# Kernel optimization log

Hardware: AMD Instinct MI355X
Metric: run time of the kernel (lower is better)

The kernel has to match this reference:

```python
import jax, jax.numpy as jnp
import numpy as np

D_MODEL = 1024
N_HEAD = 16
B, T = 4, 2048


def setup_inputs() -> dict:
    key = jax.random.key(0)
    k1, k2, k3, k4, k5 = jax.random.split(key, 5)
    s = 0.02
    return {
        "x": jax.random.normal(k1, (B, T, D_MODEL), dtype=jnp.float32),
        "w_attn": jax.random.normal(k2, (3 * D_MODEL, D_MODEL), dtype=jnp.float32) * s,
        "b_attn": jax.random.normal(k3, (3 * D_MODEL,), dtype=jnp.float32) * s,
        "w_proj": jax.random.normal(k4, (D_MODEL, D_MODEL), dtype=jnp.float32) * s,
        "b_proj": jax.random.normal(k5, (D_MODEL,), dtype=jnp.float32) * s,
    }


def reference(x, w_attn, b_attn, w_proj, b_proj):
    # x: [B, T, C]
    Bb, Tt, C = x.shape
    H = N_HEAD
    dk = C // H
    scale = 1.0 / np.sqrt(dk).astype(np.float32)

    qkv = x @ w_attn.T + b_attn                      # [B, T, 3C]
    q, k, v = jnp.split(qkv, 3, axis=-1)             # each [B, T, C]
    # -> [B, H, T, dk]
    q = q.reshape(Bb, Tt, H, dk).transpose(0, 2, 1, 3)
    k = k.reshape(Bb, Tt, H, dk).transpose(0, 2, 1, 3)
    v = v.reshape(Bb, Tt, H, dk).transpose(0, 2, 1, 3)

    att = jnp.einsum("bhqd,bhkd->bhqk", q, k) * scale   # [B, H, T, T]
    att = jax.nn.softmax(att, axis=-1)
    y = jnp.einsum("bhqk,bhkd->bhqd", att, v)            # [B, H, T, dk]
    y = y.transpose(0, 2, 1, 3).reshape(Bb, Tt, C)       # [B, T, C]
    return y @ w_proj.T + b_proj
```

## Files before the change

### kernel.cpp

```cpp
#include <hip/hip_runtime.h>
#include <hip/hip_bf16.h>

typedef __attribute__((ext_vector_type(8))) short short8;
typedef __attribute__((ext_vector_type(4))) float floatx4;
typedef __attribute__((ext_vector_type(16))) float floatx16;

#define B_ 4
#define T_ 2048
#define C_ 1024
#define H_ 16
#define DK_ 64
#define M_ (B_ * T_)
#define N3_ (3 * C_)

#define QSCALE 0.1803368801111243f

__device__ __forceinline__ unsigned short f2bf(float f) {
    union { float f; unsigned u; } v; v.f = f;
    unsigned r = v.u + 0x7fffu + ((v.u >> 16) & 1u);
    return (unsigned short)(r >> 16);
}
__device__ __forceinline__ unsigned fbits(float f) {
    union { float f; unsigned u; } v; v.f = f; return v.u;
}
__device__ __forceinline__ unsigned pack_bf16(float a, float b) {
#if __has_builtin(__builtin_amdgcn_cvt_pk_bf16_f32)
    typedef __attribute__((ext_vector_type(2))) __bf16 bf16x2;
    bf16x2 r = __builtin_amdgcn_cvt_pk_bf16_f32(a, b);
    union { bf16x2 v; unsigned u; } c; c.v = r; return c.u;
#else
    return __builtin_amdgcn_perm(fbits(b) + 0x8000u, fbits(a) + 0x8000u, 0x07060302u);
#endif
}

__device__ __forceinline__ void gload_lds16(const unsigned short* g, unsigned short* l) {
    __builtin_amdgcn_global_load_lds(
        (const __attribute__((address_space(1))) unsigned int*)(const void*)g,
        (__attribute__((address_space(3))) unsigned int*)(void*)l, 16, 0, 0);
}

#define NX4 (M_ * C_ / 4)
#define NA4 (N3_ * C_ / 4)
#define NP4 (C_ * C_ / 4)
__global__ __launch_bounds__(256) void cast3_kernel(const float* __restrict__ x,
                                                    const float* __restrict__ wa,
                                                    const float* __restrict__ wp,
                                                    unsigned short* __restrict__ xb,
                                                    unsigned short* __restrict__ wab,
                                                    unsigned short* __restrict__ wpb) {
    int i = blockIdx.x * 256 + threadIdx.x;
    const float* src; unsigned short* dst; int j;
    if (i < NX4) { src = x; dst = xb; j = i; }
    else if (i < NX4 + NA4) { src = wa; dst = wab; j = i - NX4; }
    else { src = wp; dst = wpb; j = i - NX4 - NA4; }
    float4 v = ((const float4*)src)[j];
    ushort4 o;
    o.x = f2bf(v.x); o.y = f2bf(v.y); o.z = f2bf(v.z); o.w = f2bf(v.w);
    ((ushort4*)dst)[j] = o;
}

#define BM 128
#define BN 128
#define BK 32

__global__ __launch_bounds__(256) void gemm_qkv(const unsigned short* __restrict__ A,
                                                const unsigned short* __restrict__ W,
                                                const float* __restrict__ bias,
                                                unsigned short* __restrict__ qout,
                                                unsigned short* __restrict__ kout,
                                                unsigned short* __restrict__ vout) {
    const int Kd = C_;
    __shared__ unsigned short As[BM * BK];
    __shared__ unsigned short Bs[BN * BK];
    int m0 = blockIdx.y * BM;
    int n0 = blockIdx.x * BN;
    int tid = threadIdx.x;
    int lane = tid & 63, w = tid >> 6;
    int wm = (w >> 1) * 64, wn = (w & 1) * 64;
    int l16 = lane & 15, quad = lane >> 4;
    int r4 = lane >> 2, c4 = (lane & 3) * 8;

    floatx4 acc[4][4] = {};
    for (int kt = 0; kt < Kd; kt += BK) {
        __syncthreads();
        for (int t = 0; t < 2; ++t) {
            int rbase = w * 32 + t * 16;
            gload_lds16(&A[(size_t)(m0 + rbase + r4) * Kd + kt + c4], &As[rbase * BK]);
            gload_lds16(&W[(size_t)(n0 + rbase + r4) * Kd + kt + c4], &Bs[rbase * BK]);
        }
        __syncthreads();
        short8 af[4], bf[4];
        for (int i = 0; i < 4; ++i)
            af[i] = *(const short8*)&As[(wm + 16 * i + l16) * BK + quad * 8];
        for (int j = 0; j < 4; ++j)
            bf[j] = *(const short8*)&Bs[(wn + 16 * j + l16) * BK + quad * 8];
        for (int i = 0; i < 4; ++i)
            for (int j = 0; j < 4; ++j)
                acc[i][j] = __builtin_amdgcn_mfma_f32_16x16x32_bf16(af[i], bf[j], acc[i][j], 0, 0, 0);
    }
    for (int i = 0; i < 4; ++i)
        for (int j = 0; j < 4; ++j) {
            int col = n0 + wn + 16 * j + l16;
            float bval = bias[col];
            int sec = col >> 10, cc = col & 1023;
            int h = cc >> 6, d = cc & 63;
            float qs = (sec == 0) ? QSCALE : 1.0f;
            unsigned short* dst = (sec == 0) ? qout : ((sec == 1) ? kout : vout);
            for (int r = 0; r < 4; ++r) {
                int m = m0 + wm + 16 * i + quad * 4 + r;
                int b = m >> 11, t = m & (T_ - 1);
                int bh = b * H_ + h;
                dst[((size_t)bh * T_ + t) * DK_ + d] = f2bf((acc[i][j][r] + bval) * qs);
            }
        }
}

__global__ __launch_bounds__(256) void gemm_proj(const unsigned short* __restrict__ A,
                                                 const unsigned short* __restrict__ W,
                                                 const float* __restrict__ bias,
                                                 float* __restrict__ out) {
    const int Kd = C_;
    __shared__ unsigned short As[BM * BK];
    __shared__ unsigned short Bs[BN * BK];
    int m0 = blockIdx.y * BM;
    int n0 = blockIdx.x * BN;
    int tid = threadIdx.x;
    int lane = tid & 63, w = tid >> 6;
    int wm = (w >> 1) * 64, wn = (w & 1) * 64;
    int l16 = lane & 15, quad = lane >> 4;
    int r4 = lane >> 2, c4 = (lane & 3) * 8;

    floatx4 acc[4][4] = {};
    for (int kt = 0; kt < Kd; kt += BK) {
        __syncthreads();
        for (int t = 0; t < 2; ++t) {
            int rbase = w * 32 + t * 16;
            gload_lds16(&A[(size_t)(m0 + rbase + r4) * Kd + kt + c4], &As[rbase * BK]);
            gload_lds16(&W[(size_t)(n0 + rbase + r4) * Kd + kt + c4], &Bs[rbase * BK]);
        }
        __syncthreads();
        short8 af[4], bf[4];
        for (int i = 0; i < 4; ++i)
            af[i] = *(const short8*)&As[(wm + 16 * i + l16) * BK + quad * 8];
        for (int j = 0; j < 4; ++j)
            bf[j] = *(const short8*)&Bs[(wn + 16 * j + l16) * BK + quad * 8];
        for (int i = 0; i < 4; ++i)
            for (int j = 0; j < 4; ++j)
                acc[i][j] = __builtin_amdgcn_mfma_f32_16x16x32_bf16(af[i], bf[j], acc[i][j], 0, 0, 0);
    }
    for (int i = 0; i < 4; ++i)
        for (int j = 0; j < 4; ++j) {
            int col = n0 + wn + 16 * j + l16;
            float bval = bias[col];
            for (int r = 0; r < 4; ++r) {
                int m = m0 + wm + 16 * i + quad * 4 + r;
                out[(size_t)m * C_ + col] = acc[i][j][r] + bval;
            }
        }
}

#define TLD 258
__global__ __launch_bounds__(256) void vtrans_kernel(const unsigned short* __restrict__ V,
                                                     unsigned short* __restrict__ Vt) {
    __shared__ unsigned short L[64 * TLD];
    int bid = blockIdx.x;
    int t0 = (bid & 7) * 256;
    int bh = bid >> 3;
    int tid = threadIdx.x;
    const unsigned short* src = V + ((size_t)bh * T_ + t0) * DK_;
    unsigned short* dst = Vt + (size_t)bh * DK_ * T_ + t0;
    for (int it = 0; it < 8; ++it) {
        int t = it * 32 + (tid >> 3);
        int dseg = (tid & 7) * 8;
        short8 v = *(const short8*)&src[(size_t)t * DK_ + dseg];
        for (int j = 0; j < 8; ++j)
            L[(dseg + j) * TLD + t] = ((unsigned short*)&v)[j];
    }
    __syncthreads();
    for (int it = 0; it < 8; ++it) {
        int d = it * 8 + (tid >> 5);
        int toff = (tid & 31) * 8;
        short8 r = *(const short8*)&L[d * TLD + toff];
        *(short8*)&dst[(size_t)d * T_ + toff] = r;
    }
}

#define KT 64
#define LD 72

__global__ __launch_bounds__(256, 2) void attn_kernel(const unsigned short* __restrict__ Q,
                                                      const unsigned short* __restrict__ Kv,
                                                      const unsigned short* __restrict__ Vt,
                                                      unsigned short* __restrict__ Y) {
    __shared__ unsigned short Ks[KT * LD];
    __shared__ unsigned short Vts[DK_ * LD];
    __shared__ unsigned short Ps[256 * LD];

    int bid = blockIdx.x;
    int qt = bid & 7;
    int bh = bid >> 3;
    int b = bh >> 4, hh = bh & 15;
    const unsigned short* qh = Q + (size_t)bh * T_ * DK_;
    const unsigned short* kh = Kv + (size_t)bh * T_ * DK_;
    const unsigned short* vtg = Vt + (size_t)bh * DK_ * T_;

    int tid = threadIdx.x, lane = tid & 63, w = tid >> 6;
    int l31 = lane & 31, h = lane >> 5;
    int qrA = qt * 256 + w * 32;
    int qrB = qrA + 128;

    short8 qfA[4], qfB[4];
    for (int c = 0; c < 4; ++c) {
        qfA[c] = *(const short8*)&qh[(size_t)(qrA + l31) * DK_ + 16 * c + 8 * h];
        qfB[c] = *(const short8*)&qh[(size_t)(qrB + l31) * DK_ + 16 * c + 8 * h];
    }

    floatx16 oA0 = {}, oA1 = {}, oB0 = {}, oB1 = {};
    float lA = 0.f, lB = 0.f;

    unsigned short* Pw = &Ps[w * 64 * LD];

    for (int kt = 0; kt < T_; kt += KT) {
        __syncthreads();
        for (int it = 0; it < 2; ++it) {
            int idx = tid + it * 256;
            int r8 = idx >> 3, c8 = (idx & 7) * 8;
            *(short8*)&Ks[r8 * LD + c8] = *(const short8*)&kh[(size_t)(kt + r8) * DK_ + c8];
            *(short8*)&Vts[r8 * LD + c8] = *(const short8*)&vtg[(size_t)r8 * T_ + kt + c8];
        }
        __syncthreads();

        floatx16 sA0 = {}, sA1 = {}, sB0 = {}, sB1 = {};
        for (int c = 0; c < 4; ++c) {
            short8 kf0 = *(const short8*)&Ks[l31 * LD + 16 * c + 8 * h];
            short8 kf1 = *(const short8*)&Ks[(32 + l31) * LD + 16 * c + 8 * h];
            sA0 = __builtin_amdgcn_mfma_f32_32x32x16_bf16(kf0, qfA[c], sA0, 0, 0, 0);
            sA1 = __builtin_amdgcn_mfma_f32_32x32x16_bf16(kf1, qfA[c], sA1, 0, 0, 0);
            sB0 = __builtin_amdgcn_mfma_f32_32x32x16_bf16(kf0, qfB[c], sB0, 0, 0, 0);
            sB1 = __builtin_amdgcn_mfma_f32_32x32x16_bf16(kf1, qfB[c], sB1, 0, 0, 0);
        }

        {
            float ts = 0.f;
            for (int a = 0; a < 4; ++a) {
                float p0 = __builtin_amdgcn_exp2f(sA0[4 * a + 0]);
                float p1 = __builtin_amdgcn_exp2f(sA0[4 * a + 1]);
                float p2 = __builtin_amdgcn_exp2f(sA0[4 * a + 2]);
                float p3 = __builtin_amdgcn_exp2f(sA0[4 * a + 3]);
                ts += (p0 + p1) + (p2 + p3);
                uint2 u = { pack_bf16(p0, p1), pack_bf16(p2, p3) };
                *(uint2*)&Pw[l31 * LD + 8 * a + 4 * h] = u;
            }
            for (int a = 0; a < 4; ++a) {
                float p0 = __builtin_amdgcn_exp2f(sA1[4 * a + 0]);
                float p1 = __builtin_amdgcn_exp2f(sA1[4 * a + 1]);
                float p2 = __builtin_amdgcn_exp2f(sA1[4 * a + 2]);
                float p3 = __builtin_amdgcn_exp2f(sA1[4 * a + 3]);
                ts += (p0 + p1) + (p2 + p3);
                uint2 u = { pack_bf16(p0, p1), pack_bf16(p2, p3) };
                *(uint2*)&Pw[l31 * LD + 32 + 8 * a + 4 * h] = u;
            }
            lA += ts;
        }
        {
            float ts = 0.f;
            for (int a = 0; a < 4; ++a) {
                float p0 = __builtin_amdgcn_exp2f(sB0[4 * a + 0]);
                float p1 = __builtin_amdgcn_exp2f(sB0[4 * a + 1]);
                float p2 = __builtin_amdgcn_exp2f(sB0[4 * a + 2]);
                float p3 = __builtin_amdgcn_exp2f(sB0[4 * a + 3]);
                ts += (p0 + p1) + (p2 + p3);
                uint2 u = { pack_bf16(p0, p1), pack_bf16(p2, p3) };
                *(uint2*)&Pw[(32 + l31) * LD + 8 * a + 4 * h] = u;
            }
            for (int a = 0; a < 4; ++a) {
                float p0 = __builtin_amdgcn_exp2f(sB1[4 * a + 0]);
                float p1 = __builtin_amdgcn_exp2f(sB1[4 * a + 1]);
                float p2 = __builtin_amdgcn_exp2f(sB1[4 * a + 2]);
                float p3 = __builtin_amdgcn_exp2f(sB1[4 * a + 3]);
                ts += (p0 + p1) + (p2 + p3);
                uint2 u = { pack_bf16(p0, p1), pack_bf16(p2, p3) };
                *(uint2*)&Pw[(32 + l31) * LD + 32 + 8 * a + 4 * h] = u;
            }
            lB += ts;
        }

        for (int c = 0; c < 4; ++c) {
            short8 vf0 = *(const short8*)&Vts[l31 * LD + 16 * c + 8 * h];
            short8 vf1 = *(const short8*)&Vts[(32 + l31) * LD + 16 * c + 8 * h];
            short8 pfA = *(const short8*)&Pw[l31 * LD + 16 * c + 8 * h];
            short8 pfB = *(const short8*)&Pw[(32 + l31) * LD + 16 * c + 8 * h];
            oA0 = __builtin_amdgcn_mfma_f32_32x32x16_bf16(vf0, pfA, oA0, 0, 0, 0);
            oA1 = __builtin_amdgcn_mfma_f32_32x32x16_bf16(vf1, pfA, oA1, 0, 0, 0);
            oB0 = __builtin_amdgcn_mfma_f32_32x32x16_bf16(vf0, pfB, oB0, 0, 0, 0);
            oB1 = __builtin_amdgcn_mfma_f32_32x32x16_bf16(vf1, pfB, oB1, 0, 0, 0);
        }
    }

    float invA = 1.0f / (lA + __shfl_xor(lA, 32, 64));
    float invB = 1.0f / (lB + __shfl_xor(lB, 32, 64));
    __syncthreads();
    for (int a = 0; a < 4; ++a) {
        ushort4 u;
        u.x = f2bf(oA0[4 * a + 0] * invA); u.y = f2bf(oA0[4 * a + 1] * invA);
        u.z = f2bf(oA0[4 * a + 2] * invA); u.w = f2bf(oA0[4 * a + 3] * invA);
        *(ushort4*)&Ps[(w * 32 + l31) * LD + 8 * a + 4 * h] = u;
        ushort4 v;
        v.x = f2bf(oA1[4 * a + 0] * invA); v.y = f2bf(oA1[4 * a + 1] * invA);
        v.z = f2bf(oA1[4 * a + 2] * invA); v.w = f2bf(oA1[4 * a + 3] * invA);
        *(ushort4*)&Ps[(w * 32 + l31) * LD + 32 + 8 * a + 4 * h] = v;
        ushort4 x;
        x.x = f2bf(oB0[4 * a + 0] * invB); x.y = f2bf(oB0[4 * a + 1] * invB);
        x.z = f2bf(oB0[4 * a + 2] * invB); x.w = f2bf(oB0[4 * a + 3] * invB);
        *(ushort4*)&Ps[(128 + w * 32 + l31) * LD + 8 * a + 4 * h] = x;
        ushort4 y;
        y.x = f2bf(oB1[4 * a + 0] * invB); y.y = f2bf(oB1[4 * a + 1] * invB);
        y.z = f2bf(oB1[4 * a + 2] * invB); y.w = f2bf(oB1[4 * a + 3] * invB);
        *(ushort4*)&Ps[(128 + w * 32 + l31) * LD + 32 + 8 * a + 4 * h] = y;
    }
    __syncthreads();
    int q_l = tid >> 1, seg = tid & 1;
    for (int pass = 0; pass < 2; ++pass) {
        int r = pass * 128 + q_l;
        const unsigned short* srcp = &Ps[(size_t)r * LD + seg * 32];
        unsigned short* dstp = &Y[((size_t)b * T_ + qt * 256 + r) * C_ + hh * DK_ + seg * 32];
        for (int j = 0; j < 4; ++j)
            *(short8*)&dstp[8 * j] = *(const short8*)&srcp[8 * j];
    }
}

extern "C" void kernel_launch(void* const* d_in, const int* in_sizes, int n_in,
                              void* d_out, int out_size, void* d_ws, size_t ws_size,
                              hipStream_t stream) {
    const float* x      = (const float*)d_in[0];
    const float* w_attn = (const float*)d_in[1];
    const float* b_attn = (const float*)d_in[2];
    const float* w_proj = (const float*)d_in[3];
    const float* b_proj = (const float*)d_in[4];
    float* out = (float*)d_out;

    unsigned short* ws = (unsigned short*)d_ws;
    unsigned short* xb  = ws;
    unsigned short* wab = xb  + (size_t)M_ * C_;
    unsigned short* wpb = wab + (size_t)N3_ * C_;
    unsigned short* qb  = wpb + (size_t)C_ * C_;
    unsigned short* kb  = qb  + (size_t)M_ * C_;
    unsigned short* vb  = kb  + (size_t)M_ * C_;
    unsigned short* yb  = vb  + (size_t)M_ * C_;
    unsigned short* vtb = xb;

    cast3_kernel<<<(NX4 + NA4 + NP4) / 256, 256, 0, stream>>>(x, w_attn, w_proj, xb, wab, wpb);
    gemm_qkv<<<dim3(N3_ / BN, M_ / BM), 256, 0, stream>>>(xb, wab, b_attn, qb, kb, vb);
    vtrans_kernel<<<B_ * H_ * (T_ / 256), 256, 0, stream>>>(vb, vtb);
    attn_kernel<<<B_ * H_ * (T_ / 256), 256, 0, stream>>>(qb, kb, vtb, yb);
    gemm_proj<<<dim3(C_ / BN, M_ / BM), 256, 0, stream>>>(yb, wpb, b_proj, out);
}
```

Baseline: 278.4 us.

## Keep softmax probabilities in registers as MFMA operands, shrink attention LDS

The exponentiated scores are packed to bf16 in registers and fed straight into the PV MFMA as the B operand, instead of going through an LDS round trip. V fragments are read with a permuted k-index so the contraction order matches the register layout of the score accumulator. Shared memory drops from K+V+P buffers to a single 128-row buffer reused for the output epilogue, written in two halves. This cuts LDS traffic and footprint, which may allow more resident blocks, at the cost of more live registers and split 8-byte V loads.

```diff
diff --git a/kernel.cpp b/kernel.cpp
--- a/kernel.cpp
+++ b/kernel.cpp
@@ -2,6 +2,7 @@
 #include <hip/hip_bf16.h>
 
 typedef __attribute__((ext_vector_type(8))) short short8;
+typedef __attribute__((ext_vector_type(4))) short short4v;
 typedef __attribute__((ext_vector_type(4))) float floatx4;
 typedef __attribute__((ext_vector_type(16))) float floatx16;
 
@@ -192,9 +193,9 @@
                                                       const unsigned short* __restrict__ Kv,
                                                       const unsigned short* __restrict__ Vt,
                                                       unsigned short* __restrict__ Y) {
-    __shared__ unsigned short Ks[KT * LD];
-    __shared__ unsigned short Vts[DK_ * LD];
-    __shared__ unsigned short Ps[256 * LD];
+    __shared__ unsigned short smem[128 * LD];
+    unsigned short* Ks = smem;
+    unsigned short* Vts = smem + 64 * LD;
 
     int bid = blockIdx.x;
     int qt = bid & 7;
@@ -217,8 +218,6 @@
 
     floatx16 oA0 = {}, oA1 = {}, oB0 = {}, oB1 = {};
     float lA = 0.f, lB = 0.f;
-
-    unsigned short* Pw = &Ps[w * 64 * LD];
 
     for (int kt = 0; kt < T_; kt += KT) {
         __syncthreads();
@@ -240,90 +239,82 @@
             sB1 = __builtin_amdgcn_mfma_f32_32x32x16_bf16(kf1, qfB[c], sB1, 0, 0, 0);
         }
 
-        {
-            float ts = 0.f;
-            for (int a = 0; a < 4; ++a) {
-                float p0 = __builtin_amdgcn_exp2f(sA0[4 * a + 0]);
-                float p1 = __builtin_amdgcn_exp2f(sA0[4 * a + 1]);
-                float p2 = __builtin_amdgcn_exp2f(sA0[4 * a + 2]);
-                float p3 = __builtin_amdgcn_exp2f(sA0[4 * a + 3]);
-                ts += (p0 + p1) + (p2 + p3);
-                uint2 u = { pack_bf16(p0, p1), pack_bf16(p2, p3) };
-                *(uint2*)&Pw[l31 * LD + 8 * a + 4 * h] = u;
+        unsigned pA[16], pB[16];
+        float tsA = 0.f, tsB = 0.f;
+        for (int r2 = 0; r2 < 8; ++r2) {
+            float a0 = __builtin_amdgcn_exp2f(sA0[2 * r2]);
+            float a1 = __builtin_amdgcn_exp2f(sA0[2 * r2 + 1]);
+            tsA += a0 + a1; pA[r2] = pack_bf16(a0, a1);
+            float a2 = __builtin_amdgcn_exp2f(sA1[2 * r2]);
+            float a3 = __builtin_amdgcn_exp2f(sA1[2 * r2 + 1]);
+            tsA += a2 + a3; pA[8 + r2] = pack_bf16(a2, a3);
+            float b0 = __builtin_amdgcn_exp2f(sB0[2 * r2]);
+            float b1 = __builtin_amdgcn_exp2f(sB0[2 * r2 + 1]);
+            tsB += b0 + b1; pB[r2] = pack_bf16(b0, b1);
+            float b2 = __builtin_amdgcn_exp2f(sB1[2 * r2]);
+            float b3 = __builtin_amdgcn_exp2f(sB1[2 * r2 + 1]);
+            tsB += b2 + b3; pB[8 + r2] = pack_bf16(b2, b3);
+        }
+        lA += tsA; lB += tsB;
+
+        for (int c = 0; c < 4; ++c) {
+            short8 vf0, vf1;
+            {
+                short4v lo0 = *(const short4v*)&Vts[l31 * LD + 16 * c + 4 * h];
+                short4v hi0 = *(const short4v*)&Vts[l31 * LD + 16 * c + 8 + 4 * h];
+                short4v lo1 = *(const short4v*)&Vts[(32 + l31) * LD + 16 * c + 4 * h];
+                short4v hi1 = *(const short4v*)&Vts[(32 + l31) * LD + 16 * c + 8 + 4 * h];
+                for (int j = 0; j < 4; ++j) {
+                    vf0[j] = lo0[j]; vf0[4 + j] = hi0[j];
+                    vf1[j] = lo1[j]; vf1[4 + j] = hi1[j];
+                }
             }
-            for (int a = 0; a < 4; ++a) {
-                float p0 = __builtin_amdgcn_exp2f(sA1[4 * a + 0]);
-                float p1 = __builtin_amdgcn_exp2f(sA1[4 * a + 1]);
-                float p2 = __builtin_amdgcn_exp2f(sA1[4 * a + 2]);
-                float p3 = __builtin_amdgcn_exp2f(sA1[4 * a + 3]);
-                ts += (p0 + p1) + (p2 + p3);
-                uint2 u = { pack_bf16(p0, p1), pack_bf16(p2, p3) };
-                *(uint2*)&Pw[l31 * LD + 32 + 8 * a + 4 * h] = u;
-            }
-            lA += ts;
-        }
-        {
-            float ts = 0.f;
-            for (int a = 0; a < 4; ++a) {
-                float p0 = __builtin_amdgcn_exp2f(sB0[4 * a + 0]);
-                float p1 = __builtin_amdgcn_exp2f(sB0[4 * a + 1]);
-                float p2 = __builtin_amdgcn_exp2f(sB0[4 * a + 2]);
-                float p3 = __builtin_amdgcn_exp2f(sB0[4 * a + 3]);
-                ts += (p0 + p1) + (p2 + p3);
-                uint2 u = { pack_bf16(p0, p1), pack_bf16(p2, p3) };
-                *(uint2*)&Pw[(32 + l31) * LD + 8 * a + 4 * h] = u;
-            }
-            for (int a = 0; a < 4; ++a) {
-                float p0 = __builtin_amdgcn_exp2f(sB1[4 * a + 0]);
-                float p1 = __builtin_amdgcn_exp2f(sB1[4 * a + 1]);
-                float p2 = __builtin_amdgcn_exp2f(sB1[4 * a + 2]);
-                float p3 = __builtin_amdgcn_exp2f(sB1[4 * a + 3]);
-                ts += (p0 + p1) + (p2 + p3);
-                uint2 u = { pack_bf16(p0, p1), pack_bf16(p2, p3) };
-                *(uint2*)&Pw[(32 + l31) * LD + 32 + 8 * a + 4 * h] = u;
-            }
-            lB += ts;
-        }
-
-        for (int c = 0; c < 4; ++c) {
-            short8 vf0 = *(const short8*)&Vts[l31 * LD + 16 * c + 8 * h];
-            short8 vf1 = *(const short8*)&Vts[(32 + l31) * LD + 16 * c + 8 * h];
-            short8 pfA = *(const short8*)&Pw[l31 * LD + 16 * c + 8 * h];
-            short8 pfB = *(const short8*)&Pw[(32 + l31) * LD + 16 * c + 8 * h];
-            oA0 = __builtin_amdgcn_mfma_f32_32x32x16_bf16(vf0, pfA, oA0, 0, 0, 0);
-            oA1 = __builtin_amdgcn_mfma_f32_32x32x16_bf16(vf1, pfA, oA1, 0, 0, 0);
-            oB0 = __builtin_amdgcn_mfma_f32_32x32x16_bf16(vf0, pfB, oB0, 0, 0, 0);
-            oB1 = __builtin_amdgcn_mfma_f32_32x32x16_bf16(vf1, pfB, oB1, 0, 0, 0);
+            union { unsigned u[4]; short8 s; } fA, fB;
+            for (int j = 0; j < 4; ++j) { fA.u[j] = pA[4 * c + j]; fB.u[j] = pB[4 * c + j]; }
+            oA0 = __builtin_amdgcn_mfma_f32_32x32x16_bf16(vf0, fA.s, oA0, 0, 0, 0);
+            oA1 = __builtin_amdgcn_mfma_f32_32x32x16_bf16(vf1, fA.s, oA1, 0, 0, 0);
+            oB0 = __builtin_amdgcn_mfma_f32_32x32x16_bf16(vf0, fB.s, oB0, 0, 0, 0);
+            oB1 = __builtin_amdgcn_mfma_f32_32x32x16_bf16(vf1, fB.s, oB1, 0, 0, 0);
         }
     }
 
     float invA = 1.0f / (lA + __shfl_xor(lA, 32, 64));
     float invB = 1.0f / (lB + __shfl_xor(lB, 32, 64));
+    int q_l = tid >> 1, seg = tid & 1;
+
     __syncthreads();
     for (int a = 0; a < 4; ++a) {
         ushort4 u;
         u.x = f2bf(oA0[4 * a + 0] * invA); u.y = f2bf(oA0[4 * a + 1] * invA);
         u.z = f2bf(oA0[4 * a + 2] * invA); u.w = f2bf(oA0[4 * a + 3] * invA);
-        *(ushort4*)&Ps[(w * 32 + l31) * LD + 8 * a + 4 * h] = u;
+        *(ushort4*)&smem[(w * 32 + l31) * LD + 8 * a + 4 * h] = u;
         ushort4 v;
         v.x = f2bf(oA1[4 * a + 0] * invA); v.y = f2bf(oA1[4 * a + 1] * invA);
         v.z = f2bf(oA1[4 * a + 2] * invA); v.w = f2bf(oA1[4 * a + 3] * invA);
-        *(ushort4*)&Ps[(w * 32 + l31) * LD + 32 + 8 * a + 4 * h] = v;
-        ushort4 x;
-        x.x = f2bf(oB0[4 * a + 0] * invB); x.y = f2bf(oB0[4 * a + 1] * invB);
-        x.z = f2bf(oB0[4 * a + 2] * invB); x.w = f2bf(oB0[4 * a + 3] * invB);
-        *(ushort4*)&Ps[(128 + w * 32 + l31) * LD + 8 * a + 4 * h] = x;
-        ushort4 y;
-        y.x = f2bf(oB1[4 * a + 0] * invB); y.y = f2bf(oB1[4 * a + 1] * invB);
-        y.z = f2bf(oB1[4 * a + 2] * invB); y.w = f2bf(oB1[4 * a + 3] * invB);
-        *(ushort4*)&Ps[(128 + w * 32 + l31) * LD + 32 + 8 * a + 4 * h] = y;
-    }
-    __syncthreads();
-    int q_l = tid >> 1, seg = tid & 1;
-    for (int pass = 0; pass < 2; ++pass) {
-        int r = pass * 128 + q_l;
-        const unsigned short* srcp = &Ps[(size_t)r * LD + seg * 32];
-        unsigned short* dstp = &Y[((size_t)b * T_ + qt * 256 + r) * C_ + hh * DK_ + seg * 32];
+        *(ushort4*)&smem[(w * 32 + l31) * LD + 32 + 8 * a + 4 * h] = v;
+    }
+    __syncthreads();
+    {
+        const unsigned short* srcp = &smem[(size_t)q_l * LD + seg * 32];
+        unsigned short* dstp = &Y[((size_t)b * T_ + qt * 256 + q_l) * C_ + hh * DK_ + seg * 32];
+        for (int j = 0; j < 4; ++j)
+            *(short8*)&dstp[8 * j] = *(const short8*)&srcp[8 * j];
+    }
+    __syncthreads();
+    for (int a = 0; a < 4; ++a) {
+        ushort4 u;
+        u.x = f2bf(oB0[4 * a + 0] * invB); u.y = f2bf(oB0[4 * a + 1] * invB);
+        u.z = f2bf(oB0[4 * a + 2] * invB); u.w = f2bf(oB0[4 * a + 3] * invB);
+        *(ushort4*)&smem[(w * 32 + l31) * LD + 8 * a + 4 * h] = u;
+        ushort4 v;
+        v.x = f2bf(oB1[4 * a + 0] * invB); v.y = f2bf(oB1[4 * a + 1] * invB);
+        v.z = f2bf(oB1[4 * a + 2] * invB); v.w = f2bf(oB1[4 * a + 3] * invB);
+        *(ushort4*)&smem[(w * 32 + l31) * LD + 32 + 8 * a + 4 * h] = v;
+    }
+    __syncthreads();
+    {
+        const unsigned short* srcp = &smem[(size_t)q_l * LD + seg * 32];
+        unsigned short* dstp = &Y[((size_t)b * T_ + qt * 256 + 128 + q_l) * C_ + hh * DK_ + seg * 32];
         for (int j = 0; j < 4; ++j)
             *(short8*)&dstp[8 * j] = *(const short8*)&srcp[8 * j];
     }
```

Result: faster. 269.7 us (-3.1%).
